# Kernel tuning notes

Measured on AMD Instinct MI355X. Metric: run time of the kernel, lower is better.

The kernel has to match this reference:

```python
import jax, jax.numpy as jnp
import numpy as np

WEIGHT = 1e-7       # lambda for the CRF loss
SIGMA_RGB = 15.0    # color-similarity bandwidth
SIGMA_XY = 100.0    # spatial-proximity bandwidth
SCALE = 0.5         # scale_factor (sigma_xy is multiplied by it in forward)


def setup_inputs() -> dict:
    key = jax.random.key(0)
    k1, k2 = jax.random.split(key)
    images = jax.random.uniform(k1, (4, 3, 128, 128), jnp.float32) * 255.0  # [0,255] RGB
    logits = jax.random.normal(k2, (4, 4, 128, 128), jnp.float32)
    segmentations = jax.nn.softmax(logits, axis=1)  # softmaxed logits, N*K*H*W
    return {"images": images, "segmentations": segmentations}


def _crf_loss(images, segmentations):
    n, k, h, w = segmentations.shape
    # F.interpolate(images, scale_factor=0.5, mode='nearest') == stride-2 subsample
    img_s = images[:, :, ::2, ::2]
    # F.interpolate(segs, scale_factor=0.5, mode='bilinear', align_corners=False)
    # for exact /2 downscale == 2x2 average pooling
    hs, ws = h // 2, w // 2
    seg_s = segmentations.reshape(n, k, hs, 2, ws, 2).mean(axis=(3, 5))  # [n,k,hs,ws]

    P = hs * ws
    yy, xx = jnp.meshgrid(jnp.arange(hs, dtype=jnp.float32),
                          jnp.arange(ws, dtype=jnp.float32), indexing='ij')
    sigma_xy_eff = SIGMA_XY * SCALE
    pos = jnp.stack([xx, yy], axis=-1).reshape(P, 2) / sigma_xy_eff      # [P,2]
    rgb = img_s.reshape(n, 3, P).transpose(0, 2, 1) / SIGMA_RGB          # [n,P,3]
    feats = jnp.concatenate([jnp.broadcast_to(pos[None], (n, P, 2)), rgb], axis=-1)  # [n,P,5]

    # exact dense Gaussian bilateral kernel W_ij = exp(-0.5*||f_i - f_j||^2)
    sq = jnp.sum(feats * feats, axis=-1)                                 # [n,P]
    d2 = sq[:, :, None] + sq[:, None, :] - 2.0 * jnp.einsum('npc,nqc->npq', feats, feats)
    Wk = jnp.exp(-0.5 * jnp.maximum(d2, 0.0))                            # [n,P,P]

    S = seg_s.reshape(n, k, P)
    AS = jnp.einsum('npq,nkq->nkp', Wk, S)                               # bilateral-filtered segs
    loss = -jnp.sum(S * AS) / jnp.float32(n)
    return (WEIGHT * loss).reshape(1)


def reference(images, segmentations):
    return _crf_loss(images, segmentations)
```

## Files before the change

kernel.cpp:

```cpp
#include <hip/hip_runtime.h>

#define NB   4
#define KCH  4
#define P    4096
#define REC  12
#define QT   64
#define BLK  256
#define PT   2
#define NPT  8
#define NBLK 288

#if __has_builtin(__builtin_amdgcn_exp2f)
#define EXPFN(x) __builtin_amdgcn_exp2f(x)
#define FSCALE 1.2011224087864498f
#else
#define EXPFN(x) __expf(x)
#define FSCALE 1.0f
#endif

__device__ __forceinline__ void make_rec(const float* __restrict__ images,
                                         const float* __restrict__ segs,
                                         int n, int p, float* o ) {
    int i = p >> 6;
    int j = p & 63;
    int off = 256 * i + 2 * j;
    const float* img = images + (size_t)n * 3 * 16384;
    float x = (float)j * (FSCALE / 50.0f);
    float y = (float)i * (FSCALE / 50.0f);
    float r = img[0 * 16384 + off] * (FSCALE / 15.0f);
    float g = img[1 * 16384 + off] * (FSCALE / 15.0f);
    float b = img[2 * 16384 + off] * (FSCALE / 15.0f);
    float h = -0.5f * (x * x + y * y + r * r + g * g + b * b);
    o[0] = x; o[1] = y; o[2] = r; o[3] = g; o[4] = b; o[5] = h;
    const float* sg = segs + (size_t)n * KCH * 16384;
#pragma unroll
    for (int k = 0; k < KCH; ++k) {
        float2 s0 = *(const float2*)(sg + k * 16384 + off);
        float2 s1 = *(const float2*)(sg + k * 16384 + off + 128);
        o[6 + k] = 0.25f * ((s0.x + s0.y) + (s1.x + s1.y));
    }
}

__global__ __launch_bounds__(256) void crf_fused(const float* __restrict__ images,
                                                 const float* __restrict__ segs,
                                                 float* __restrict__ out) {
    __shared__ float lds[QT * REC];
    __shared__ float wsum[BLK / 64];

    int t = threadIdx.x;
    int n = blockIdx.y;

    static const int cum[NPT] = {0, 64, 120, 168, 208, 240, 264, 280};
    int b = blockIdx.x;
    int pt = 0;
#pragma unroll
    for (int i = 1; i < NPT; ++i) pt += (b >= cum[i]) ? 1 : 0;
    int qc = b - cum[pt] + 8 * pt;
    int pbase = pt * (BLK * PT);
    int qbase = qc * QT;
    bool mixed = (qc >> 3) == pt;

    if (t < QT) {
        float o[10];
        make_rec(images, segs, n, qbase + t, o);
        float* l = lds + t * REC;
        *(float4*)(l + 0) = make_float4(o[0], o[1], o[2], o[3]);
        *(float4*)(l + 4) = make_float4(o[4], o[5], o[6], o[7]);
        *(float2*)(l + 8) = make_float2(o[8], o[9]);
    }

    float rp[PT][10];
#pragma unroll
    for (int pi = 0; pi < PT; ++pi)
        make_rec(images, segs, n, pbase + t + pi * BLK, rp[pi]);
    __syncthreads();

    float acc[PT] = {0.f, 0.f};
    float acc_all;

    if (!mixed) {
#pragma unroll 4
        for (int q = 0; q < QT; ++q) {
            const float4* rq = (const float4*)(lds + q * REC);
            float4 f0 = rq[0];
            float4 f1 = rq[1];
            float4 f2 = rq[2];
#pragma unroll
            for (int pi = 0; pi < PT; ++pi) {
                float d = rp[pi][5] + f1.y;
                d = fmaf(rp[pi][0], f0.x, d);
                d = fmaf(rp[pi][1], f0.y, d);
                d = fmaf(rp[pi][2], f0.z, d);
                d = fmaf(rp[pi][3], f0.w, d);
                d = fmaf(rp[pi][4], f1.x, d);
                float w = EXPFN(d);
                float sd = rp[pi][6] * f1.z;
                sd = fmaf(rp[pi][7], f1.w, sd);
                sd = fmaf(rp[pi][8], f2.x, sd);
                sd = fmaf(rp[pi][9], f2.y, sd);
                acc[pi] = fmaf(w, sd, acc[pi]);
            }
        }
        acc_all = 2.0f * (acc[0] + acc[1]);
    } else {
#pragma unroll 4
        for (int q = 0; q < QT; ++q) {
            const float4* rq = (const float4*)(lds + q * REC);
            float4 f0 = rq[0];
            float4 f1 = rq[1];
            float4 f2 = rq[2];
            int qg = qbase + q;
#pragma unroll
            for (int pi = 0; pi < PT; ++pi) {
                int pg = pbase + t + pi * BLK;
                float d = rp[pi][5] + f1.y;
                d = fmaf(rp[pi][0], f0.x, d);
                d = fmaf(rp[pi][1], f0.y, d);
                d = fmaf(rp[pi][2], f0.z, d);
                d = fmaf(rp[pi][3], f0.w, d);
                d = fmaf(rp[pi][4], f1.x, d);
                float w = EXPFN(d);
                float sd = rp[pi][6] * f1.z;
                sd = fmaf(rp[pi][7], f1.w, sd);
                sd = fmaf(rp[pi][8], f2.x, sd);
                sd = fmaf(rp[pi][9], f2.y, sd);
                float f = (qg > pg) ? 2.0f : ((qg == pg) ? 1.0f : 0.0f);
                acc[pi] = fmaf(w, sd * f, acc[pi]);
            }
        }
        acc_all = acc[0] + acc[1];
    }

#pragma unroll
    for (int off = 32; off > 0; off >>= 1)
        acc_all += __shfl_down(acc_all, off, 64);
    if ((t & 63) == 0) wsum[t >> 6] = acc_all;
    __syncthreads();
    if (t == 0) {
        float s = (wsum[0] + wsum[1]) + (wsum[2] + wsum[3]);
        atomicAdd(out, s * (-2.5e-8f));
    }
}

extern "C" void kernel_launch(void* const* d_in, const int* in_sizes, int n_in,
                              void* d_out, int out_size, void* d_ws, size_t ws_size,
                              hipStream_t stream) {
    const float* images = (const float*)d_in[0];
    const float* segs   = (const float*)d_in[1];
    float* out = (float*)d_out;
    (void)d_ws; (void)ws_size;

    (void)hipMemsetAsync(out, 0, sizeof(float), stream);
    crf_fused<<<dim3(NBLK, NB), dim3(256), 0, stream>>>(images, segs, out);
}
```

Before: 76.80 us.

## Split feature prep into separate kernel and read q-records from global instead of LDS

Per-pixel feature records (position, color, norm term, pooled segmentation) are now computed once by a prep kernel and written to workspace buffers in a struct-of-arrays layout. The pair kernel then loads its p-records and streams q-records directly from global memory, using uniform addresses, instead of rebuilding them from the images and staging them in LDS. This removes redundant recomputation, the LDS staging and the __syncthreads barrier. In exchange it adds a second kernel launch and a workspace round-trip, and the inner loop now depends on global or scalar loads.

```diff
diff --git a/kernel.cpp b/kernel.cpp
--- a/kernel.cpp
+++ b/kernel.cpp
@@ -2,8 +2,7 @@
 
 #define NB   4
 #define KCH  4
-#define P    4096
-#define REC  12
+#define PPB  4096
 #define QT   64
 #define BLK  256
 #define PT   2
@@ -18,117 +17,150 @@
 #define FSCALE 1.0f
 #endif
 
-__device__ __forceinline__ void make_rec(const float* __restrict__ images,
-                                         const float* __restrict__ segs,
-                                         int n, int p, float* o ) {
+
+__global__ __launch_bounds__(256) void crf_prep(const float* __restrict__ images,
+                                                const float* __restrict__ segs,
+                                                float4* __restrict__ RA,
+                                                float4* __restrict__ RB,
+                                                float2* __restrict__ RC) {
+    int gid = blockIdx.x * BLK + threadIdx.x;
+    int n = gid >> 12;
+    int p = gid & (PPB - 1);
     int i = p >> 6;
     int j = p & 63;
     int off = 256 * i + 2 * j;
     const float* img = images + (size_t)n * 3 * 16384;
     float x = (float)j * (FSCALE / 50.0f);
     float y = (float)i * (FSCALE / 50.0f);
-    float r = img[0 * 16384 + off] * (FSCALE / 15.0f);
-    float g = img[1 * 16384 + off] * (FSCALE / 15.0f);
-    float b = img[2 * 16384 + off] * (FSCALE / 15.0f);
+    float r = img[off]         * (FSCALE / 15.0f);
+    float g = img[16384 + off] * (FSCALE / 15.0f);
+    float b = img[32768 + off] * (FSCALE / 15.0f);
     float h = -0.5f * (x * x + y * y + r * r + g * g + b * b);
-    o[0] = x; o[1] = y; o[2] = r; o[3] = g; o[4] = b; o[5] = h;
     const float* sg = segs + (size_t)n * KCH * 16384;
-#pragma unroll
-    for (int k = 0; k < KCH; ++k) {
-        float2 s0 = *(const float2*)(sg + k * 16384 + off);
-        float2 s1 = *(const float2*)(sg + k * 16384 + off + 128);
-        o[6 + k] = 0.25f * ((s0.x + s0.y) + (s1.x + s1.y));
+    float s0, s1, s2, s3;
+    {
+        float2 u0 = *(const float2*)(sg + off);
+        float2 u1 = *(const float2*)(sg + off + 128);
+        s0 = 0.25f * ((u0.x + u0.y) + (u1.x + u1.y));
+        u0 = *(const float2*)(sg + 16384 + off);
+        u1 = *(const float2*)(sg + 16384 + off + 128);
+        s1 = 0.25f * ((u0.x + u0.y) + (u1.x + u1.y));
+        u0 = *(const float2*)(sg + 32768 + off);
+        u1 = *(const float2*)(sg + 32768 + off + 128);
+        s2 = 0.25f * ((u0.x + u0.y) + (u1.x + u1.y));
+        u0 = *(const float2*)(sg + 49152 + off);
+        u1 = *(const float2*)(sg + 49152 + off + 128);
+        s3 = 0.25f * ((u0.x + u0.y) + (u1.x + u1.y));
     }
+    RA[gid] = make_float4(x, y, r, g);
+    RB[gid] = make_float4(b, h, s0, s1);
+    RC[gid] = make_float2(s2, s3);
 }
 
-__global__ __launch_bounds__(256) void crf_fused(const float* __restrict__ images,
-                                                 const float* __restrict__ segs,
+__global__ __launch_bounds__(256) void crf_pairs(const float4* __restrict__ RA,
+                                                 const float4* __restrict__ RB,
+                                                 const float2* __restrict__ RC,
                                                  float* __restrict__ out) {
-    __shared__ float lds[QT * REC];
     __shared__ float wsum[BLK / 64];
-
     int t = threadIdx.x;
     int n = blockIdx.y;
 
-    static const int cum[NPT] = {0, 64, 120, 168, 208, 240, 264, 280};
     int b = blockIdx.x;
     int pt = 0;
-#pragma unroll
-    for (int i = 1; i < NPT; ++i) pt += (b >= cum[i]) ? 1 : 0;
-    int qc = b - cum[pt] + 8 * pt;
+    pt += (b >= 64); pt += (b >= 120); pt += (b >= 168); pt += (b >= 208);
+    pt += (b >= 240); pt += (b >= 264); pt += (b >= 280);
+    int qc = b - pt * (60 - 4 * pt);
     int pbase = pt * (BLK * PT);
     int qbase = qc * QT;
     bool mixed = (qc >> 3) == pt;
+    int base = n << 12;
 
-    if (t < QT) {
-        float o[10];
-        make_rec(images, segs, n, qbase + t, o);
-        float* l = lds + t * REC;
-        *(float4*)(l + 0) = make_float4(o[0], o[1], o[2], o[3]);
-        *(float4*)(l + 4) = make_float4(o[4], o[5], o[6], o[7]);
-        *(float2*)(l + 8) = make_float2(o[8], o[9]);
-    }
+    float4 a0 = RA[base + pbase + t];
+    float4 a1 = RA[base + pbase + t + BLK];
+    float4 b0 = RB[base + pbase + t];
+    float4 b1 = RB[base + pbase + t + BLK];
+    float2 c0 = RC[base + pbase + t];
+    float2 c1 = RC[base + pbase + t + BLK];
 
-    float rp[PT][10];
-#pragma unroll
-    for (int pi = 0; pi < PT; ++pi)
-        make_rec(images, segs, n, pbase + t + pi * BLK, rp[pi]);
-    __syncthreads();
+    const float4* __restrict__ qA = RA + base + qbase;
+    const float4* __restrict__ qB = RB + base + qbase;
+    const float2* __restrict__ qC = RC + base + qbase;
 
-    float acc[PT] = {0.f, 0.f};
+    float acc0 = 0.f, acc1 = 0.f;
     float acc_all;
 
     if (!mixed) {
 #pragma unroll 4
         for (int q = 0; q < QT; ++q) {
-            const float4* rq = (const float4*)(lds + q * REC);
-            float4 f0 = rq[0];
-            float4 f1 = rq[1];
-            float4 f2 = rq[2];
-#pragma unroll
-            for (int pi = 0; pi < PT; ++pi) {
-                float d = rp[pi][5] + f1.y;
-                d = fmaf(rp[pi][0], f0.x, d);
-                d = fmaf(rp[pi][1], f0.y, d);
-                d = fmaf(rp[pi][2], f0.z, d);
-                d = fmaf(rp[pi][3], f0.w, d);
-                d = fmaf(rp[pi][4], f1.x, d);
-                float w = EXPFN(d);
-                float sd = rp[pi][6] * f1.z;
-                sd = fmaf(rp[pi][7], f1.w, sd);
-                sd = fmaf(rp[pi][8], f2.x, sd);
-                sd = fmaf(rp[pi][9], f2.y, sd);
-                acc[pi] = fmaf(w, sd, acc[pi]);
-            }
+            float4 fa = qA[q];
+            float4 fb = qB[q];
+            float2 fc = qC[q];
+            float d0 = b0.y + fb.y;
+            d0 = fmaf(a0.x, fa.x, d0);
+            d0 = fmaf(a0.y, fa.y, d0);
+            d0 = fmaf(a0.z, fa.z, d0);
+            d0 = fmaf(a0.w, fa.w, d0);
+            d0 = fmaf(b0.x, fb.x, d0);
+            float w0 = EXPFN(d0);
+            float sd0 = b0.z * fb.z;
+            sd0 = fmaf(b0.w, fb.w, sd0);
+            sd0 = fmaf(c0.x, fc.x, sd0);
+            sd0 = fmaf(c0.y, fc.y, sd0);
+            acc0 = fmaf(w0, sd0, acc0);
+
+            float d1 = b1.y + fb.y;
+            d1 = fmaf(a1.x, fa.x, d1);
+            d1 = fmaf(a1.y, fa.y, d1);
+            d1 = fmaf(a1.z, fa.z, d1);
+            d1 = fmaf(a1.w, fa.w, d1);
+            d1 = fmaf(b1.x, fb.x, d1);
+            float w1 = EXPFN(d1);
+            float sd1 = b1.z * fb.z;
+            sd1 = fmaf(b1.w, fb.w, sd1);
+            sd1 = fmaf(c1.x, fc.x, sd1);
+            sd1 = fmaf(c1.y, fc.y, sd1);
+            acc1 = fmaf(w1, sd1, acc1);
         }
-        acc_all = 2.0f * (acc[0] + acc[1]);
+        acc_all = 2.0f * (acc0 + acc1);
     } else {
+        int pg0 = pbase + t;
+        int pg1 = pbase + t + BLK;
 #pragma unroll 4
         for (int q = 0; q < QT; ++q) {
-            const float4* rq = (const float4*)(lds + q * REC);
-            float4 f0 = rq[0];
-            float4 f1 = rq[1];
-            float4 f2 = rq[2];
+            float4 fa = qA[q];
+            float4 fb = qB[q];
+            float2 fc = qC[q];
             int qg = qbase + q;
-#pragma unroll
-            for (int pi = 0; pi < PT; ++pi) {
-                int pg = pbase + t + pi * BLK;
-                float d = rp[pi][5] + f1.y;
-                d = fmaf(rp[pi][0], f0.x, d);
-                d = fmaf(rp[pi][1], f0.y, d);
-                d = fmaf(rp[pi][2], f0.z, d);
-                d = fmaf(rp[pi][3], f0.w, d);
-                d = fmaf(rp[pi][4], f1.x, d);
-                float w = EXPFN(d);
-                float sd = rp[pi][6] * f1.z;
-                sd = fmaf(rp[pi][7], f1.w, sd);
-                sd = fmaf(rp[pi][8], f2.x, sd);
-                sd = fmaf(rp[pi][9], f2.y, sd);
-                float f = (qg > pg) ? 2.0f : ((qg == pg) ? 1.0f : 0.0f);
-                acc[pi] = fmaf(w, sd * f, acc[pi]);
-            }
+
+            float d0 = b0.y + fb.y;
+            d0 = fmaf(a0.x, fa.x, d0);
+            d0 = fmaf(a0.y, fa.y, d0);
+            d0 = fmaf(a0.z, fa.z, d0);
+            d0 = fmaf(a0.w, fa.w, d0);
+            d0 = fmaf(b0.x, fb.x, d0);
+            float w0 = EXPFN(d0);
+            float sd0 = b0.z * fb.z;
+            sd0 = fmaf(b0.w, fb.w, sd0);
+            sd0 = fmaf(c0.x, fc.x, sd0);
+            sd0 = fmaf(c0.y, fc.y, sd0);
+            float f0 = (qg > pg0) ? 2.0f : ((qg == pg0) ? 1.0f : 0.0f);
+            acc0 = fmaf(w0, sd0 * f0, acc0);
+
+            float d1 = b1.y + fb.y;
+            d1 = fmaf(a1.x, fa.x, d1);
+            d1 = fmaf(a1.y, fa.y, d1);
+            d1 = fmaf(a1.z, fa.z, d1);
+            d1 = fmaf(a1.w, fa.w, d1);
+            d1 = fmaf(b1.x, fb.x, d1);
+            float w1 = EXPFN(d1);
+            float sd1 = b1.z * fb.z;
+            sd1 = fmaf(b1.w, fb.w, sd1);
+            sd1 = fmaf(c1.x, fc.x, sd1);
+            sd1 = fmaf(c1.y, fc.y, sd1);
+            float f1 = (qg > pg1) ? 2.0f : ((qg == pg1) ? 1.0f : 0.0f);
+            acc1 = fmaf(w1, sd1 * f1, acc1);
         }
-        acc_all = acc[0] + acc[1];
+        acc_all = acc0 + acc1;
     }
 
 #pragma unroll
@@ -148,8 +180,13 @@
     const float* images = (const float*)d_in[0];
     const float* segs   = (const float*)d_in[1];
     float* out = (float*)d_out;
-    (void)d_ws; (void)ws_size;
+    char* ws = (char*)d_ws;
+    float4* RA = (float4*)(ws);
+    float4* RB = (float4*)(ws + 262144);
+    float2* RC = (float2*)(ws + 524288);
+    (void)in_sizes; (void)n_in; (void)out_size; (void)ws_size;
 
     (void)hipMemsetAsync(out, 0, sizeof(float), stream);
-    crf_fused<<<dim3(NBLK, NB), dim3(256), 0, stream>>>(images, segs, out);
+    crf_prep<<<dim3(64), dim3(256), 0, stream>>>(images, segs, RA, RB, RC);
+    crf_pairs<<<dim3(NBLK, NB), dim3(256), 0, stream>>>(RA, RB, RC, out);
 }
```

Result: slower. 78.90 us (+2.7%).

## Compute pairwise bilateral dot products with bf16-split MFMA over triangular tiles

Applied to the files above, without the earlier changes.

Replaces the scalar FMA pairwise loop with MFMA 16x16x32 bf16 matrix ops. Features and segmentations are split into three and two bf16 parts respectively, giving cross-term products that keep close to fp32 accuracy. A prep kernel writes packed bf16 fragments and norms to workspace. The pairs kernel covers the upper triangle in 64x64 tiles and writes per-block partial sums, which a single-block kernel reduces deterministically instead of using atomics. The cost is three launches, workspace traffic, and a possible accuracy risk from the bf16 splits.

```diff
diff --git a/kernel.cpp b/kernel.cpp
--- a/kernel.cpp
+++ b/kernel.cpp
@@ -1,14 +1,10 @@
 #include <hip/hip_runtime.h>
 
-#define NB   4
-#define KCH  4
-#define P    4096
-#define REC  12
-#define QT   64
-#define BLK  256
-#define PT   2
-#define NPT  8
-#define NBLK 288
+#define NB    4
+#define PPB   4096
+#define BLK   256
+#define NBLK2 2080
+#define NPART (NBLK2 * NB)
 
 #if __has_builtin(__builtin_amdgcn_exp2f)
 #define EXPFN(x) __builtin_amdgcn_exp2f(x)
@@ -18,127 +14,194 @@
 #define FSCALE 1.0f
 #endif
 
-__device__ __forceinline__ void make_rec(const float* __restrict__ images,
-                                         const float* __restrict__ segs,
-                                         int n, int p, float* o ) {
+typedef __attribute__((ext_vector_type(8))) short short8v;
+typedef __attribute__((ext_vector_type(4))) float f32x4;
+
+typedef unsigned int uint;
+typedef unsigned short ushort;
+
+__device__ __forceinline__ ushort bsplit(float v, float& rem) {
+    uint u = __float_as_uint(v);
+    uint r = (u + 0x7FFFu + ((u >> 16) & 1u)) >> 16;
+    rem = v - __uint_as_float(r << 16);
+    return (ushort)r;
+}
+
+__global__ __launch_bounds__(256) void crf_prep(const float* __restrict__ images,
+                                                const float* __restrict__ segs,
+                                                uint* __restrict__ FA,
+                                                uint* __restrict__ FB,
+                                                uint* __restrict__ SA,
+                                                uint* __restrict__ SB,
+                                                float* __restrict__ H) {
+    int gid = blockIdx.x * BLK + threadIdx.x;
+    int n = gid >> 12;
+    int p = gid & (PPB - 1);
     int i = p >> 6;
     int j = p & 63;
     int off = 256 * i + 2 * j;
     const float* img = images + (size_t)n * 3 * 16384;
-    float x = (float)j * (FSCALE / 50.0f);
-    float y = (float)i * (FSCALE / 50.0f);
-    float r = img[0 * 16384 + off] * (FSCALE / 15.0f);
-    float g = img[1 * 16384 + off] * (FSCALE / 15.0f);
-    float b = img[2 * 16384 + off] * (FSCALE / 15.0f);
-    float h = -0.5f * (x * x + y * y + r * r + g * g + b * b);
-    o[0] = x; o[1] = y; o[2] = r; o[3] = g; o[4] = b; o[5] = h;
-    const float* sg = segs + (size_t)n * KCH * 16384;
-#pragma unroll
-    for (int k = 0; k < KCH; ++k) {
-        float2 s0 = *(const float2*)(sg + k * 16384 + off);
-        float2 s1 = *(const float2*)(sg + k * 16384 + off + 128);
-        o[6 + k] = 0.25f * ((s0.x + s0.y) + (s1.x + s1.y));
-    }
-}
-
-__global__ __launch_bounds__(256) void crf_fused(const float* __restrict__ images,
-                                                 const float* __restrict__ segs,
-                                                 float* __restrict__ out) {
-    __shared__ float lds[QT * REC];
+    float f[5];
+    f[0] = (float)j * (FSCALE / 50.0f);
+    f[1] = (float)i * (FSCALE / 50.0f);
+    f[2] = img[off]         * (FSCALE / 15.0f);
+    f[3] = img[16384 + off] * (FSCALE / 15.0f);
+    f[4] = img[32768 + off] * (FSCALE / 15.0f);
+    float h = -0.5f * (f[0]*f[0] + f[1]*f[1] + f[2]*f[2] + f[3]*f[3] + f[4]*f[4]);
+
+    const float* sg = segs + (size_t)n * 4 * 16384;
+    float s[4];
+#pragma unroll
+    for (int k = 0; k < 4; ++k) {
+        float2 u0 = *(const float2*)(sg + k * 16384 + off);
+        float2 u1 = *(const float2*)(sg + k * 16384 + off + 128);
+        s[k] = 0.25f * ((u0.x + u0.y) + (u1.x + u1.y));
+    }
+
+    ushort v[3][5];
+    ushort tg[2][4];
+#pragma unroll
+    for (int c = 0; c < 5; ++c) {
+        float r1, r2, dead;
+        v[0][c] = bsplit(f[c], r1);
+        v[1][c] = bsplit(r1, r2);
+        v[2][c] = bsplit(r2, dead);
+    }
+#pragma unroll
+    for (int c = 0; c < 4; ++c) {
+        float r1, dead;
+        tg[0][c] = bsplit(s[c], r1);
+        tg[1][c] = bsplit(r1, dead);
+    }
+
+    static const int PA[6] = {0, 0, 1, 0, 1, 2};
+    static const int PB[6] = {0, 1, 0, 2, 1, 0};
+    uint* fap = FA + (size_t)gid * 16;
+    uint* fbp = FB + (size_t)gid * 16;
+#pragma unroll
+    for (int k2 = 0; k2 < 16; ++k2) {
+        int s0 = 2 * k2, s1 = s0 + 1;
+        uint lo = (s0 >= 30) ? 0u : (uint)v[PA[s0 / 5]][s0 % 5];
+        uint hi = (s1 >= 30) ? 0u : (uint)v[PA[s1 / 5]][s1 % 5];
+        fap[k2] = lo | (hi << 16);
+        lo = (s0 >= 30) ? 0u : (uint)v[PB[s0 / 5]][s0 % 5];
+        hi = (s1 >= 30) ? 0u : (uint)v[PB[s1 / 5]][s1 % 5];
+        fbp[k2] = lo | (hi << 16);
+    }
+    static const int QA[3] = {0, 0, 1};
+    static const int QB[3] = {0, 1, 0};
+    uint* sap = SA + (size_t)gid * 16;
+    uint* sbp = SB + (size_t)gid * 16;
+#pragma unroll
+    for (int k2 = 0; k2 < 16; ++k2) {
+        int s0 = 2 * k2, s1 = s0 + 1;
+        uint lo = (s0 >= 12) ? 0u : (uint)tg[QA[s0 / 4]][s0 % 4];
+        uint hi = (s1 >= 12) ? 0u : (uint)tg[QA[s1 / 4]][s1 % 4];
+        sap[k2] = lo | (hi << 16);
+        lo = (s0 >= 12) ? 0u : (uint)tg[QB[s0 / 4]][s0 % 4];
+        hi = (s1 >= 12) ? 0u : (uint)tg[QB[s1 / 4]][s1 % 4];
+        sbp[k2] = lo | (hi << 16);
+    }
+    H[gid] = h;
+}
+
+__global__ __launch_bounds__(256, 6) void crf_pairs(const uint4* __restrict__ FA,
+                                                    const uint4* __restrict__ FB,
+                                                    const uint4* __restrict__ SA,
+                                                    const uint4* __restrict__ SB,
+                                                    const float* __restrict__ H,
+                                                    float* __restrict__ part) {
     __shared__ float wsum[BLK / 64];
-
     int t = threadIdx.x;
     int n = blockIdx.y;
-
-    static const int cum[NPT] = {0, 64, 120, 168, 208, 240, 264, 280};
+    int lane = t & 63;
+    int w = t >> 6;
+    int l15 = lane & 15;
+    int lhi = lane >> 4;
+
     int b = blockIdx.x;
-    int pt = 0;
-#pragma unroll
-    for (int i = 1; i < NPT; ++i) pt += (b >= cum[i]) ? 1 : 0;
-    int qc = b - cum[pt] + 8 * pt;
-    int pbase = pt * (BLK * PT);
-    int qbase = qc * QT;
-    bool mixed = (qc >> 3) == pt;
-
-    if (t < QT) {
-        float o[10];
-        make_rec(images, segs, n, qbase + t, o);
-        float* l = lds + t * REC;
-        *(float4*)(l + 0) = make_float4(o[0], o[1], o[2], o[3]);
-        *(float4*)(l + 4) = make_float4(o[4], o[5], o[6], o[7]);
-        *(float2*)(l + 8) = make_float2(o[8], o[9]);
-    }
-
-    float rp[PT][10];
-#pragma unroll
-    for (int pi = 0; pi < PT; ++pi)
-        make_rec(images, segs, n, pbase + t + pi * BLK, rp[pi]);
-    __syncthreads();
-
-    float acc[PT] = {0.f, 0.f};
-    float acc_all;
-
-    if (!mixed) {
-#pragma unroll 4
-        for (int q = 0; q < QT; ++q) {
-            const float4* rq = (const float4*)(lds + q * REC);
-            float4 f0 = rq[0];
-            float4 f1 = rq[1];
-            float4 f2 = rq[2];
-#pragma unroll
-            for (int pi = 0; pi < PT; ++pi) {
-                float d = rp[pi][5] + f1.y;
-                d = fmaf(rp[pi][0], f0.x, d);
-                d = fmaf(rp[pi][1], f0.y, d);
-                d = fmaf(rp[pi][2], f0.z, d);
-                d = fmaf(rp[pi][3], f0.w, d);
-                d = fmaf(rp[pi][4], f1.x, d);
-                float w = EXPFN(d);
-                float sd = rp[pi][6] * f1.z;
-                sd = fmaf(rp[pi][7], f1.w, sd);
-                sd = fmaf(rp[pi][8], f2.x, sd);
-                sd = fmaf(rp[pi][9], f2.y, sd);
-                acc[pi] = fmaf(w, sd, acc[pi]);
+    int pc = 0;
+#pragma unroll
+    for (int i = 1; i < 64; ++i) pc += (b >= (64 * i - (i * (i - 1)) / 2)) ? 1 : 0;
+    int qc = b - (64 * pc - (pc * (pc - 1)) / 2) + pc;
+    bool diagblk = (pc == qc);
+    int base = n << 12;
+    int prow0 = pc * 64 + w * 16;
+
+    size_t arow = (size_t)(base + prow0 + l15) * 4 + lhi;
+    short8v afrag = __builtin_bit_cast(short8v, FA[arow]);
+    short8v safrag = __builtin_bit_cast(short8v, SA[arow]);
+    float hp[4];
+#pragma unroll
+    for (int r = 0; r < 4; ++r)
+        hp[r] = H[base + prow0 + lhi * 4 + r];
+
+    float accP = 0.f;
+    float accD = 0.f;
+
+#pragma unroll
+    for (int jj = 0; jj < 4; ++jj) {
+        if (diagblk && jj < w) continue;
+        int qrow0 = qc * 64 + jj * 16;
+        size_t brow = (size_t)(base + qrow0 + l15) * 4 + lhi;
+        short8v bfrag = __builtin_bit_cast(short8v, FB[brow]);
+        short8v sbfrag = __builtin_bit_cast(short8v, SB[brow]);
+        float hq = H[base + qrow0 + l15];
+
+        f32x4 cf = {0.f, 0.f, 0.f, 0.f};
+        f32x4 cs = {0.f, 0.f, 0.f, 0.f};
+        cf = __builtin_amdgcn_mfma_f32_16x16x32_bf16(afrag, bfrag, cf, 0, 0, 0);
+        cs = __builtin_amdgcn_mfma_f32_16x16x32_bf16(safrag, sbfrag, cs, 0, 0, 0);
+
+        if (diagblk && jj == w) {
+#pragma unroll
+            for (int r = 0; r < 4; ++r) {
+                float d = cf[r] + (hp[r] + hq);
+                float wg = EXPFN(d);
+                int pg = lhi * 4 + r;
+                float fw = (l15 > pg) ? 2.0f : ((l15 == pg) ? 1.0f : 0.0f);
+                accD = fmaf(wg * fw, cs[r], accD);
+            }
+        } else {
+#pragma unroll
+            for (int r = 0; r < 4; ++r) {
+                float d = cf[r] + (hp[r] + hq);
+                float wg = EXPFN(d);
+                accP = fmaf(wg, cs[r], accP);
             }
         }
-        acc_all = 2.0f * (acc[0] + acc[1]);
-    } else {
-#pragma unroll 4
-        for (int q = 0; q < QT; ++q) {
-            const float4* rq = (const float4*)(lds + q * REC);
-            float4 f0 = rq[0];
-            float4 f1 = rq[1];
-            float4 f2 = rq[2];
-            int qg = qbase + q;
-#pragma unroll
-            for (int pi = 0; pi < PT; ++pi) {
-                int pg = pbase + t + pi * BLK;
-                float d = rp[pi][5] + f1.y;
-                d = fmaf(rp[pi][0], f0.x, d);
-                d = fmaf(rp[pi][1], f0.y, d);
-                d = fmaf(rp[pi][2], f0.z, d);
-                d = fmaf(rp[pi][3], f0.w, d);
-                d = fmaf(rp[pi][4], f1.x, d);
-                float w = EXPFN(d);
-                float sd = rp[pi][6] * f1.z;
-                sd = fmaf(rp[pi][7], f1.w, sd);
-                sd = fmaf(rp[pi][8], f2.x, sd);
-                sd = fmaf(rp[pi][9], f2.y, sd);
-                float f = (qg > pg) ? 2.0f : ((qg == pg) ? 1.0f : 0.0f);
-                acc[pi] = fmaf(w, sd * f, acc[pi]);
-            }
-        }
-        acc_all = acc[0] + acc[1];
-    }
-
+    }
+
+    float acc_all = 2.0f * accP + accD;
 #pragma unroll
     for (int off = 32; off > 0; off >>= 1)
         acc_all += __shfl_down(acc_all, off, 64);
     if ((t & 63) == 0) wsum[t >> 6] = acc_all;
     __syncthreads();
     if (t == 0) {
-        float s = (wsum[0] + wsum[1]) + (wsum[2] + wsum[3]);
-        atomicAdd(out, s * (-2.5e-8f));
+        part[n * NBLK2 + blockIdx.x] =
+            (wsum[0] + wsum[1]) + (wsum[2] + wsum[3]);
+    }
+}
+
+__global__ __launch_bounds__(256) void crf_reduce(const float* __restrict__ part,
+                                                  float* __restrict__ out) {
+    __shared__ float wsum[BLK / 64];
+    int t = threadIdx.x;
+    float s = 0.f;
+#pragma unroll
+    for (int i = 0; i < 33; ++i) {
+        int idx = t + i * BLK;
+        if (idx < NPART) s += part[idx];
+    }
+#pragma unroll
+    for (int off = 32; off > 0; off >>= 1)
+        s += __shfl_down(s, off, 64);
+    if ((t & 63) == 0) wsum[t >> 6] = s;
+    __syncthreads();
+    if (t == 0) {
+        float tot = (wsum[0] + wsum[1]) + (wsum[2] + wsum[3]);
+        out[0] = tot * (-2.5e-8f);
     }
 }
 
@@ -148,8 +211,17 @@
     const float* images = (const float*)d_in[0];
     const float* segs   = (const float*)d_in[1];
     float* out = (float*)d_out;
-    (void)d_ws; (void)ws_size;
-
-    (void)hipMemsetAsync(out, 0, sizeof(float), stream);
-    crf_fused<<<dim3(NBLK, NB), dim3(256), 0, stream>>>(images, segs, out);
-}
+    char* ws = (char*)d_ws;
+    uint* FA = (uint*)(ws);
+    uint* FB = (uint*)(ws + (1u << 20));
+    uint* SA = (uint*)(ws + (2u << 20));
+    uint* SB = (uint*)(ws + (3u << 20));
+    float* H = (float*)(ws + (4u << 20));
+    float* part = (float*)(ws + (4u << 20) + 65536);
+    (void)in_sizes; (void)n_in; (void)out_size; (void)ws_size;
+
+    crf_prep<<<dim3(64), dim3(256), 0, stream>>>(images, segs, FA, FB, SA, SB, H);
+    crf_pairs<<<dim3(NBLK2, NB), dim3(256), 0, stream>>>(
+        (const uint4*)FA, (const uint4*)FB, (const uint4*)SA, (const uint4*)SB, H, part);
+    crf_reduce<<<dim3(1), dim3(256), 0, stream>>>(part, out);
+}
```

After: 87.25 us. 13.6% more time.
